# Performance work log

Measured on AMD Instinct MI355X. Metric: run time of the kernel, lower is better.

Reference implementation:

```python
import jax, jax.numpy as jnp
import numpy as np
import jax.scipy.linalg

BATCH = 1048576
M_NUM = 2
DT = 0.0166667
NN_RATIO = 0.5
SLOPE = 0.01  # torch LeakyReLU default negative_slope


def setup_inputs() -> dict:
    key = jax.random.key(0)
    ks = jax.random.split(key, 16)
    inp = {}
    inp["SS"] = jax.random.normal(ks[0], (BATCH, 2), dtype=jnp.float32)
    inp["Alphas"] = jax.random.uniform(ks[1], (BATCH, M_NUM), dtype=jnp.float32)
    # per-muscle scalar parameters (positive so sqrt(K*I) is valid)
    inp["K0s"] = jax.random.uniform(ks[2], (M_NUM,), minval=0.5, maxval=1.5)
    inp["K1s"] = jax.random.uniform(ks[3], (M_NUM,), minval=0.5, maxval=1.5)
    inp["L0s"] = jax.random.uniform(ks[4], (M_NUM,), minval=0.5, maxval=1.5)
    inp["L1s"] = jax.random.uniform(ks[5], (M_NUM,), minval=0.1, maxval=0.6)
    inp["Ms"] = jnp.array([1.0, -1.0], dtype=jnp.float32)  # moment arms
    inp["I_p"] = jnp.array([1.0], dtype=jnp.float32)
    inp["B_p"] = jnp.array([0.05], dtype=jnp.float32)
    inp["K_p"] = jnp.array([1.0], dtype=jnp.float32)
    # per-muscle compensational MLP weights: 3-32-32-32-1 (eval mode, dropout off)
    s = 0.1
    inp["W1"] = jax.random.normal(ks[6], (M_NUM, 3, 32)) * s
    inp["b1"] = jax.random.normal(ks[7], (M_NUM, 32)) * s
    inp["W2"] = jax.random.normal(ks[8], (M_NUM, 32, 32)) * s
    inp["b2"] = jax.random.normal(ks[9], (M_NUM, 32)) * s
    inp["W3"] = jax.random.normal(ks[10], (M_NUM, 32, 32)) * s
    inp["b3"] = jax.random.normal(ks[11], (M_NUM, 32)) * s
    inp["W4"] = jax.random.normal(ks[12], (M_NUM, 32, 1)) * s
    inp["b4"] = jax.random.normal(ks[13], (M_NUM, 1)) * s
    return inp


def _leaky(x):
    return jnp.where(x >= 0, x, SLOPE * x)


def reference(SS, Alphas, K0s, K1s, L0s, L1s, Ms, I_p, B_p, K_p,
              W1, b1, W2, b2, W3, b3, W4, b4):
    B = SS.shape[0]
    a = jnp.clip(Alphas, 0.0, 1.0)                      # (B, m)
    # muscle length / speed via scalar moment arms
    l = SS[:, 0:1] * Ms[None, :]                        # (B, m)
    dl = SS[:, 1:2] * Ms[None, :]                       # (B, m)
    # compensational MLPs, vectorized over muscles
    x = jnp.stack([l, dl, a], axis=-1)                  # (B, m, 3)
    h = _leaky(jnp.einsum('bmi,mio->bmo', x, W1) + b1[None])
    h = _leaky(jnp.einsum('bmi,mio->bmo', h, W2) + b2[None])
    h = _leaky(jnp.einsum('bmi,mio->bmo', h, W3) + b3[None])
    nn_out = jnp.tanh(jnp.einsum('bmi,mio->bmo', h, W4) + b4[None])[..., 0] * NN_RATIO  # (B, m)

    I0, B0p, K0p = I_p[0], B_p[0], K_p[0]
    K_m = K0s[None, :] + K1s[None, :] * a               # (B, m)
    K_tot = jnp.sum(K_m * Ms[None, :] ** 2, axis=1)     # (B,)
    A10 = -(K_tot + K0p) / I0
    D = 2.0 * jnp.sqrt(K_tot * I0)
    A11 = -(D + B0p) / I0
    B_F = K_m * (L0s[None, :] + L1s[None, :] * a - jnp.abs(l)) \
        + K1s[None, :] * L1s[None, :] * a * a * nn_out   # (B, m)
    B10 = jnp.sum(B_F * Ms[None, :], axis=1) / I0       # (B,)

    # Build block matrix M6 = [[A*dt, B*dt, 0], [0, 0, I2], [0, 0, 0]]
    M6 = jnp.zeros((B, 6, 6), dtype=SS.dtype)
    M6 = M6.at[:, 0, 1].set(DT)
    M6 = M6.at[:, 1, 0].set(A10 * DT)
    M6 = M6.at[:, 1, 1].set(A11 * DT)
    M6 = M6.at[:, 1, 2].set(B10 * DT)
    M6 = M6.at[:, 1, 3].set(DT / I0)
    M6 = M6.at[:, 2, 4].set(1.0)
    M6 = M6.at[:, 3, 5].set(1.0)

    expMT = jax.vmap(jax.scipy.linalg.expm)(M6)         # (B, 6, 6)
    Ad = expMT[:, :2, :2]
    Bd1 = expMT[:, :2, 4:6]
    Bd0 = expMT[:, :2, 2:4] - Bd1
    u = jnp.array([1.0, 0.0], dtype=SS.dtype)           # U0 = U1 = [1, 0]
    SSout = (jnp.einsum('bij,bj->bi', Ad, SS)
             + jnp.einsum('bij,j->bi', Bd0, u)
             + jnp.einsum('bij,j->bi', Bd1, u))          # (B, 2)
    return SSout[:, :1], SSout
```

## Files before the change

### kernel.cpp

```cpp
#include <hip/hip_runtime.h>
#include <hip/hip_bf16.h>

#define NTHREADS 256
#define WAVES    4
#define GPW      4
#define DT_F     0.0166667f

typedef _Float16 f16x8 __attribute__((ext_vector_type(8)));
typedef _Float16 f16x4 __attribute__((ext_vector_type(4)));
typedef _Float16 f16x2 __attribute__((ext_vector_type(2)));
typedef float    f32x4 __attribute__((ext_vector_type(4)));

#define BF16_PROBE 0xBF803F80u

#define A1T 0
#define A4T 1024
#define B2T 2048
#define B3T 3072
#define A2T 4096
#define A3T 6144
#define SMH_F16 8192

__device__ __forceinline__ float leaky(float x) { return fmaxf(x, 0.01f * x); }

__device__ __forceinline__ float tanh_fast(float x) {
    const float xc = fminf(fmaxf(x, -10.0f), 10.0f);
    const float t  = __expf(2.0f * xc);
    return (t - 1.0f) * __builtin_amdgcn_rcpf(t + 1.0f);
}

__device__ __forceinline__ f16x2 pkrtz(float a, float b) {
    return __builtin_bit_cast(f16x2, __builtin_amdgcn_cvt_pkrtz(a, b));
}

__device__ __forceinline__ f16x4 leaky_cvt(const f32x4 D) {
    f16x2 lo = pkrtz(D[0], D[1]);
    f16x2 hi = pkrtz(D[2], D[3]);
    const f16x2 sl = {(_Float16)0.01f, (_Float16)0.01f};
    lo = __builtin_elementwise_max(lo, lo * sl);
    hi = __builtin_elementwise_max(hi, hi * sl);
    return __builtin_shufflevector(lo, hi, 0, 1, 2, 3);
}

__device__ __forceinline__ f16x4 bias_leaky_cvt(const f32x4 D, const f16x4 b) {
    f16x2 lo = pkrtz(D[0], D[1]);
    f16x2 hi = pkrtz(D[2], D[3]);
    const f16x2 blo = {b[0], b[1]};
    const f16x2 bhi = {b[2], b[3]};
    lo = lo + blo;
    hi = hi + bhi;
    const f16x2 sl = {(_Float16)0.01f, (_Float16)0.01f};
    lo = __builtin_elementwise_max(lo, lo * sl);
    hi = __builtin_elementwise_max(hi, hi * sl);
    return __builtin_shufflevector(lo, hi, 0, 1, 2, 3);
}

__device__ __forceinline__ f16x8 concat8(const f16x4 a, const f16x4 b) {
    return __builtin_shufflevector(a, b, 0, 1, 2, 3, 4, 5, 6, 7);
}

__device__ __forceinline__ f32x4 mfma16(f16x4 a, f16x4 b, f32x4 c) {
    f32x4 d;
    asm("v_mfma_f32_16x16x16_f16 %0, %1, %2, %3"
        : "=&v"(d) : "v"(a), "v"(b), "v"(c));
    return d;
}
__device__ __forceinline__ f32x4 mfma32(f16x8 a, f16x8 b, f32x4 c) {
    f32x4 d;
    asm("v_mfma_f32_16x16x32_f16 %0, %1, %2, %3"
        : "=&v"(d) : "v"(a), "v"(b), "v"(c));
    return d;
}

__device__ __forceinline__ f16x4 ldsv4(const _Float16* p) {
    return *(const f16x4*)p;
}
__device__ __forceinline__ f16x8 ldsv8(const _Float16* p) {
    return *(const f16x8*)p;
}

__device__ __forceinline__ void epilogue_math(
    const float* P, float ss0, float ss1, float a0, float a1,
    float nn0, float nn1, float& o0f, float& o1f)
{
    const float K00 = P[0], K01 = P[1], K10 = P[2], K11 = P[3];
    const float L00 = P[4], L01 = P[5], L10 = P[6], L11 = P[7];
    const float Ms0 = P[8], Ms1 = P[9];
    const float I0  = P[10], B0p = P[11], K0p = P[12];

    const float Km0   = fmaf(K10, a0, K00);
    const float Km1   = fmaf(K11, a1, K01);
    const float K_tot = Km0*Ms0*Ms0 + Km1*Ms1*Ms1;
    const float invI  = 1.0f / I0;
    const float A10   = -(K_tot + K0p) * invI;
    const float Dd    = 2.0f * sqrtf(K_tot * I0);
    const float A11   = -(Dd + B0p) * invI;
    const float absl0 = fabsf(ss0 * Ms0);
    const float absl1 = fabsf(ss0 * Ms1);
    const float BF0   = Km0 * (L00 + L10*a0 - absl0) + K10*L10*a0*a0*nn0;
    const float BF1   = Km1 * (L01 + L11*a1 - absl1) + K11*L11*a1*a1*nn1;
    const float B10   = (BF0*Ms0 + BF1*Ms1) * invI;

    const float t01 = DT_F;
    const float t10 = A10 * DT_F;
    const float t11 = A11 * DT_F;

    float p00 = 1.0f/120.0f, p01 = 0.0f, p10 = 0.0f, p11 = 1.0f/120.0f;
    const float coef[4] = {1.0f/24.0f, 1.0f/6.0f, 0.5f, 1.0f};
    #pragma unroll
    for (int j = 0; j < 4; ++j) {
        const float cj  = coef[j];
        const float n00 = p01*t10 + cj;
        const float n01 = p00*t01 + p01*t11;
        const float n10 = p11*t10;
        const float n11 = p10*t01 + p11*t11 + cj;
        p00 = n00; p01 = n01; p10 = n10; p11 = n11;
    }
    const float e00 = 1.0f + t01*p10;
    const float e01 = t01*p11;
    const float e10 = t10*p00 + t11*p10;
    const float e11 = 1.0f + t10*p01 + t11*p11;

    const float cscale = DT_F * B10;
    o0f = fmaf(e00, ss0, fmaf(e01, ss1, p01 * cscale));
    o1f = fmaf(e10, ss0, fmaf(e11, ss1, p11 * cscale));
}

__device__ __forceinline__ float ldb(const __hip_bfloat16* p, int i) {
    return __bfloat162float(p[i]);
}

__device__ void run_bf16_fallback(
    const void* SSv, const void* ALv, const void* K0sv, const void* K1sv,
    const void* L0sv, const void* L1sv, const void* Msv, const void* I_pv,
    const void* B_pv, const void* K_pv, const void* W1v, const void* b1v,
    const void* W2v, const void* b2v, const void* W3v, const void* b3v,
    const void* W4v, const void* b4v, void* outv, int batch)
{
    const __hip_bfloat16* SS = (const __hip_bfloat16*)SSv;
    const __hip_bfloat16* AL = (const __hip_bfloat16*)ALv;
    const __hip_bfloat16* W1 = (const __hip_bfloat16*)W1v;
    const __hip_bfloat16* b1 = (const __hip_bfloat16*)b1v;
    const __hip_bfloat16* W2 = (const __hip_bfloat16*)W2v;
    const __hip_bfloat16* b2 = (const __hip_bfloat16*)b2v;
    const __hip_bfloat16* W3 = (const __hip_bfloat16*)W3v;
    const __hip_bfloat16* b3 = (const __hip_bfloat16*)b3v;
    const __hip_bfloat16* W4 = (const __hip_bfloat16*)W4v;
    const __hip_bfloat16* b4 = (const __hip_bfloat16*)b4v;

    float P[13];
    P[0] = ldb((const __hip_bfloat16*)K0sv, 0); P[1] = ldb((const __hip_bfloat16*)K0sv, 1);
    P[2] = ldb((const __hip_bfloat16*)K1sv, 0); P[3] = ldb((const __hip_bfloat16*)K1sv, 1);
    P[4] = ldb((const __hip_bfloat16*)L0sv, 0); P[5] = ldb((const __hip_bfloat16*)L0sv, 1);
    P[6] = ldb((const __hip_bfloat16*)L1sv, 0); P[7] = ldb((const __hip_bfloat16*)L1sv, 1);
    P[8] = ldb((const __hip_bfloat16*)Msv, 0);  P[9] = ldb((const __hip_bfloat16*)Msv, 1);
    P[10] = ldb((const __hip_bfloat16*)I_pv, 0);
    P[11] = ldb((const __hip_bfloat16*)B_pv, 0);
    P[12] = ldb((const __hip_bfloat16*)K_pv, 0);

    const int stride = gridDim.x * blockDim.x;
    for (int e = blockIdx.x * blockDim.x + threadIdx.x; e < batch; e += stride) {
        const float ss0 = ldb(SS, 2*e), ss1 = ldb(SS, 2*e+1);
        float a0 = fminf(fmaxf(ldb(AL, 2*e),   0.0f), 1.0f);
        float a1 = fminf(fmaxf(ldb(AL, 2*e+1), 0.0f), 1.0f);
        float nn[2];
        #pragma unroll 1
        for (int m = 0; m < 2; ++m) {
            const float am = m ? a1 : a0;
            const float l = ss0 * P[8+m], dl = ss1 * P[8+m];
            float h[32];
            #pragma unroll
            for (int o = 0; o < 32; ++o)
                h[o] = leaky(fmaf(l, ldb(W1, m*96+o),
                             fmaf(dl, ldb(W1, m*96+32+o),
                             fmaf(am, ldb(W1, m*96+64+o), ldb(b1, m*32+o)))));
            float g[32];
            #pragma unroll 1
            for (int oc = 0; oc < 4; ++oc) {
                float acc[8];
                #pragma unroll
                for (int j = 0; j < 8; ++j) acc[j] = ldb(b2, m*32+oc*8+j);
                #pragma unroll
                for (int k = 0; k < 32; ++k) {
                    #pragma unroll
                    for (int j = 0; j < 8; ++j)
                        acc[j] = fmaf(h[k], ldb(W2, m*1024+k*32+oc*8+j), acc[j]);
                }
                #pragma unroll
                for (int j = 0; j < 8; ++j) g[oc*8+j] = leaky(acc[j]);
            }
            float h3[32];
            #pragma unroll 1
            for (int oc = 0; oc < 4; ++oc) {
                float acc[8];
                #pragma unroll
                for (int j = 0; j < 8; ++j) acc[j] = ldb(b3, m*32+oc*8+j);
                #pragma unroll
                for (int k = 0; k < 32; ++k) {
                    #pragma unroll
                    for (int j = 0; j < 8; ++j)
                        acc[j] = fmaf(g[k], ldb(W3, m*1024+k*32+oc*8+j), acc[j]);
                }
                #pragma unroll
                for (int j = 0; j < 8; ++j) h3[oc*8+j] = leaky(acc[j]);
            }
            float acc = ldb(b4, m);
            #pragma unroll
            for (int k = 0; k < 32; ++k) acc = fmaf(h3[k], ldb(W4, m*32+k), acc);
            nn[m] = tanh_fast(acc) * 0.5f;
        }
        float o0f, o1f;
        epilogue_math(P, ss0, ss1, a0, a1, nn[0], nn[1], o0f, o1f);
        __hip_bfloat16* out0 = (__hip_bfloat16*)outv;
        __hip_bfloat162* out1 = (__hip_bfloat162*)(out0 + batch);
        out0[e] = __float2bfloat16(o0f);
        __hip_bfloat162 pr;
        pr.x = __float2bfloat16(o0f);
        pr.y = __float2bfloat16(o1f);
        out1[e] = pr;
    }
}

__global__ __launch_bounds__(NTHREADS, 4) void joint_kernel(
    const void* __restrict__ SSv, const void* __restrict__ ALv,
    const void* __restrict__ K0sv, const void* __restrict__ K1sv,
    const void* __restrict__ L0sv, const void* __restrict__ L1sv,
    const void* __restrict__ Msv,  const void* __restrict__ I_pv,
    const void* __restrict__ B_pv, const void* __restrict__ K_pv,
    const void* __restrict__ W1v,  const void* __restrict__ b1v,
    const void* __restrict__ W2v,  const void* __restrict__ b2v,
    const void* __restrict__ W3v,  const void* __restrict__ b3v,
    const void* __restrict__ W4v,  const void* __restrict__ b4v,
    void* __restrict__ outv, int batch)
{
    const unsigned probe = *(const unsigned*)Msv;
    if (probe == BF16_PROBE) {
        run_bf16_fallback(SSv, ALv, K0sv, K1sv, L0sv, L1sv, Msv, I_pv, B_pv,
                          K_pv, W1v, b1v, W2v, b2v, W3v, b3v, W4v, b4v,
                          outv, batch);
        return;
    }

    const float* SS = (const float*)SSv;
    const float* AL = (const float*)ALv;
    const float* W1 = (const float*)W1v;  const float* b1 = (const float*)b1v;
    const float* W2 = (const float*)W2v;  const float* b2 = (const float*)b2v;
    const float* W3 = (const float*)W3v;  const float* b3 = (const float*)b3v;
    const float* W4 = (const float*)W4v;  const float* b4 = (const float*)b4v;

    const int tid  = threadIdx.x;
    const int wave = tid >> 6;
    const int lane = tid & 63;
    const int n    = lane & 15;
    const int q    = lane >> 4;

    __shared__ __align__(16) _Float16 smh[SMH_F16];
    __shared__ float sb4[2];

    for (int i = tid; i < 2048; i += NTHREADS) {
        const int mi = i >> 10, rem = i & 1023, in = rem >> 5, out = rem & 31;
        const int qq = in >> 3, j = in & 7, h = (out >> 2) & 1;
        const int nn_ = ((out >> 3) << 2) | (out & 3);
        const int l  = (qq << 4) | nn_;
        smh[A2T + ((mi*2 + h)*64 + l)*8 + j] = (_Float16)W2[i];
        smh[A3T + ((mi*2 + h)*64 + l)*8 + j] = (_Float16)W3[i];
    }
    for (int i = tid; i < 1024; i += NTHREADS) {
        const int mi = i >> 9, h = (i >> 8) & 1, l = (i >> 2) & 63, j = i & 3;
        const int qq = l >> 4, nn_ = l & 15;
        const int gg = ((nn_ >> 2) << 3) + (nn_ & 3) + h*4;
        const int k  = qq*4 + j;
        float v = 0.0f;
        if (k < 3)       v = W1[mi*96 + k*32 + gg];
        else if (k == 3) v = b1[mi*32 + gg];
        smh[A1T + ((mi*2 + h)*64 + l)*4 + j] = (_Float16)v;
    }
    for (int i = tid; i < 1024; i += NTHREADS) {
        const int mi = i >> 9, l = (i >> 3) & 63, j = i & 7;
        smh[A4T + (mi*64 + l)*8 + j] = (_Float16)W4[mi*32 + (l >> 4)*8 + j];
    }
    for (int i = tid; i < 1024; i += NTHREADS) {
        const int mi = i >> 9, h = (i >> 8) & 1, l = (i >> 2) & 63, r = i & 3;
        smh[B2T + ((mi*2 + h)*64 + l)*4 + r] = (_Float16)b2[mi*32 + (l >> 4)*8 + h*4 + r];
        smh[B3T + ((mi*2 + h)*64 + l)*4 + r] = (_Float16)b3[mi*32 + (l >> 4)*8 + h*4 + r];
    }
    if (tid < 2) sb4[tid] = b4[tid];
    __syncthreads();

    f16x4 A1f[2][2], Bs2[2][2], Bs3[2][2];
    f16x8 A2f[2][2], A3f[2][2], A4f[2];
    #pragma unroll
    for (int mi = 0; mi < 2; ++mi) {
        #pragma unroll
        for (int h = 0; h < 2; ++h) {
            A1f[mi][h] = ldsv4(&smh[A1T + ((mi*2 + h)*64 + lane)*4]);
            A2f[mi][h] = ldsv8(&smh[A2T + ((mi*2 + h)*64 + lane)*8]);
            A3f[mi][h] = ldsv8(&smh[A3T + ((mi*2 + h)*64 + lane)*8]);
            Bs2[mi][h] = ldsv4(&smh[B2T + ((mi*2 + h)*64 + lane)*4]);
            Bs3[mi][h] = ldsv4(&smh[B3T + ((mi*2 + h)*64 + lane)*4]);
        }
        A4f[mi] = ldsv8(&smh[A4T + (mi*64 + lane)*8]);
    }
    const float b4s0 = sb4[0], b4s1 = sb4[1];

    float P[13];
    P[0]  = ((const float*)K0sv)[0]; P[1]  = ((const float*)K0sv)[1];
    P[2]  = ((const float*)K1sv)[0]; P[3]  = ((const float*)K1sv)[1];
    P[4]  = ((const float*)L0sv)[0]; P[5]  = ((const float*)L0sv)[1];
    P[6]  = ((const float*)L1sv)[0]; P[7]  = ((const float*)L1sv)[1];
    P[8]  = ((const float*)Msv)[0];  P[9]  = ((const float*)Msv)[1];
    P[10] = ((const float*)I_pv)[0];
    P[11] = ((const float*)B_pv)[0];
    P[12] = ((const float*)K_pv)[0];

    const f32x4 zero = {0.0f, 0.0f, 0.0f, 0.0f};
    const int groupBase = (blockIdx.x * WAVES + wave) * GPW;

    #pragma unroll 1
    for (int g = 0; g < GPW; ++g) {
        const int ebase = (groupBase + g) * 64;
        float my_r0 = 0.0f, my_r1 = 0.0f;

        float2 s0_, s1_, s2_, s3_, al0_, al1_, al2_, al3_;
        {
            const int e0 = min(ebase + 0*16 + n, batch - 1);
            const int e1 = min(ebase + 1*16 + n, batch - 1);
            const int e2 = min(ebase + 2*16 + n, batch - 1);
            const int e3 = min(ebase + 3*16 + n, batch - 1);
            s0_ = ((const float2*)SS)[e0]; al0_ = ((const float2*)AL)[e0];
            s1_ = ((const float2*)SS)[e1]; al1_ = ((const float2*)AL)[e1];
            s2_ = ((const float2*)SS)[e2]; al2_ = ((const float2*)AL)[e2];
            s3_ = ((const float2*)SS)[e3]; al3_ = ((const float2*)AL)[e3];
        }

        #pragma unroll 1
        for (int p = 0; p < 2; ++p) {
            float2 s[2], al[2];
            s[0]  = p ? s2_  : s0_;
            s[1]  = p ? s3_  : s1_;
            al[0] = p ? al2_ : al0_;
            al[1] = p ? al3_ : al1_;
            float a0c[2], a1c[2];
            #pragma unroll
            for (int ti = 0; ti < 2; ++ti) {
                a0c[ti] = fminf(fmaxf(al[ti].x, 0.0f), 1.0f);
                a1c[ti] = fminf(fmaxf(al[ti].y, 0.0f), 1.0f);
            }

            f16x4 B1[2][2];
            #pragma unroll
            for (int ti = 0; ti < 2; ++ti)
                #pragma unroll
                for (int mi = 0; mi < 2; ++mi) {
                    const float Msm = P[8 + mi];
                    const float am  = mi ? a1c[ti] : a0c[ti];
                    const f16x2 blo = pkrtz(s[ti].x * Msm, s[ti].y * Msm);
                    const f16x2 bhi = pkrtz(am, 1.0f);
                    B1[ti][mi] = __builtin_shufflevector(blo, bhi, 0, 1, 2, 3);
                }

            f16x8 Bx[2][2];
            #pragma unroll
            for (int ti = 0; ti < 2; ++ti)
                #pragma unroll
                for (int mi = 0; mi < 2; ++mi) {
                    const f32x4 d0 = mfma16(A1f[mi][0], B1[ti][mi], zero);
                    const f32x4 d1 = mfma16(A1f[mi][1], B1[ti][mi], zero);
                    Bx[ti][mi] = concat8(leaky_cvt(d0), leaky_cvt(d1));
                }
            #pragma unroll
            for (int ti = 0; ti < 2; ++ti)
                #pragma unroll
                for (int mi = 0; mi < 2; ++mi) {
                    const f32x4 d0 = mfma32(A2f[mi][0], Bx[ti][mi], zero);
                    const f32x4 d1 = mfma32(A2f[mi][1], Bx[ti][mi], zero);
                    Bx[ti][mi] = concat8(bias_leaky_cvt(d0, Bs2[mi][0]),
                                         bias_leaky_cvt(d1, Bs2[mi][1]));
                }
            #pragma unroll
            for (int ti = 0; ti < 2; ++ti)
                #pragma unroll
                for (int mi = 0; mi < 2; ++mi) {
                    const f32x4 d0 = mfma32(A3f[mi][0], Bx[ti][mi], zero);
                    const f32x4 d1 = mfma32(A3f[mi][1], Bx[ti][mi], zero);
                    Bx[ti][mi] = concat8(bias_leaky_cvt(d0, Bs3[mi][0]),
                                         bias_leaky_cvt(d1, Bs3[mi][1]));
                }
            #pragma unroll
            for (int ti = 0; ti < 2; ++ti) {
                const bool own = (q == (2*p + ti));
                #pragma unroll
                for (int mi = 0; mi < 2; ++mi) {
                    const f32x4 G = mfma32(A4f[mi], Bx[ti][mi], zero);
                    const float r = G[0] + (mi ? b4s1 : b4s0);
                    if (mi == 0) my_r0 = own ? r : my_r0;
                    else         my_r1 = own ? r : my_r1;
                }
            }
        }

        const int eo  = ebase + lane;
        const int eog = min(eo, batch - 1);
        const float2 se  = ((const float2*)SS)[eog];
        const float2 ale = ((const float2*)AL)[eog];
        const float a0 = fminf(fmaxf(ale.x, 0.0f), 1.0f);
        const float a1 = fminf(fmaxf(ale.y, 0.0f), 1.0f);
        const float nn0 = tanh_fast(my_r0) * 0.5f;
        const float nn1 = tanh_fast(my_r1) * 0.5f;
        float o0f, o1f;
        epilogue_math(P, se.x, se.y, a0, a1, nn0, nn1, o0f, o1f);
        if (eo < batch) {
            ((float*)outv)[eo] = o0f;
            ((float2*)((float*)outv + batch))[eo] = make_float2(o0f, o1f);
        }
    }
}

extern "C" void kernel_launch(void* const* d_in, const int* in_sizes, int n_in,
                              void* d_out, int out_size, void* d_ws, size_t ws_size,
                              hipStream_t stream) {
    const int batch = in_sizes[0] / 2;
    const int elemsPerBlock = 64 * GPW * WAVES;
    const int grid = (batch + elemsPerBlock - 1) / elemsPerBlock;
    joint_kernel<<<grid, NTHREADS, 0, stream>>>(
        d_in[0], d_in[1], d_in[2], d_in[3], d_in[4], d_in[5], d_in[6],
        d_in[7], d_in[8], d_in[9], d_in[10], d_in[11], d_in[12], d_in[13],
        d_in[14], d_in[15], d_in[16], d_in[17], d_out, batch);
}
```

Baseline: 121.9 us.

## Split per-muscle MLPs across wave pairs and exchange results via LDS

Each wave now evaluates the MLP for a single muscle instead of both, with pairs of waves sharing the same 64-element groups. The muscle-1 wave writes its result to a double-buffered LDS exchange, and after a block barrier the muscle-0 wave runs the epilogue and writes the output. This cuts per-wave register use (half the weight fragments), and launch bounds are raised to target higher occupancy. In exchange, the grid doubles, every block must redo the LDS weight staging, a block-wide sync is added per group, and half the waves sit idle during the epilogue.

```diff
diff --git a/kernel.cpp b/kernel.cpp
--- a/kernel.cpp
+++ b/kernel.cpp
@@ -221,7 +221,7 @@
     }
 }
 
-__global__ __launch_bounds__(NTHREADS, 4) void joint_kernel(
+__global__ __launch_bounds__(NTHREADS, 8) void joint_kernel(
     const void* __restrict__ SSv, const void* __restrict__ ALv,
     const void* __restrict__ K0sv, const void* __restrict__ K1sv,
     const void* __restrict__ L0sv, const void* __restrict__ L1sv,
@@ -253,55 +253,54 @@
     const int lane = tid & 63;
     const int n    = lane & 15;
     const int q    = lane >> 4;
+    const int mi   = wave & 1;
+    const int wp   = wave >> 1;
 
     __shared__ __align__(16) _Float16 smh[SMH_F16];
+    __shared__ float sxch[2][2][64];
     __shared__ float sb4[2];
 
     for (int i = tid; i < 2048; i += NTHREADS) {
-        const int mi = i >> 10, rem = i & 1023, in = rem >> 5, out = rem & 31;
+        const int mm = i >> 10, rem = i & 1023, in = rem >> 5, out = rem & 31;
         const int qq = in >> 3, j = in & 7, h = (out >> 2) & 1;
         const int nn_ = ((out >> 3) << 2) | (out & 3);
         const int l  = (qq << 4) | nn_;
-        smh[A2T + ((mi*2 + h)*64 + l)*8 + j] = (_Float16)W2[i];
-        smh[A3T + ((mi*2 + h)*64 + l)*8 + j] = (_Float16)W3[i];
+        smh[A2T + ((mm*2 + h)*64 + l)*8 + j] = (_Float16)W2[i];
+        smh[A3T + ((mm*2 + h)*64 + l)*8 + j] = (_Float16)W3[i];
     }
     for (int i = tid; i < 1024; i += NTHREADS) {
-        const int mi = i >> 9, h = (i >> 8) & 1, l = (i >> 2) & 63, j = i & 3;
+        const int mm = i >> 9, h = (i >> 8) & 1, l = (i >> 2) & 63, j = i & 3;
         const int qq = l >> 4, nn_ = l & 15;
         const int gg = ((nn_ >> 2) << 3) + (nn_ & 3) + h*4;
         const int k  = qq*4 + j;
         float v = 0.0f;
-        if (k < 3)       v = W1[mi*96 + k*32 + gg];
-        else if (k == 3) v = b1[mi*32 + gg];
-        smh[A1T + ((mi*2 + h)*64 + l)*4 + j] = (_Float16)v;
+        if (k < 3)       v = W1[mm*96 + k*32 + gg];
+        else if (k == 3) v = b1[mm*32 + gg];
+        smh[A1T + ((mm*2 + h)*64 + l)*4 + j] = (_Float16)v;
     }
     for (int i = tid; i < 1024; i += NTHREADS) {
-        const int mi = i >> 9, l = (i >> 3) & 63, j = i & 7;
-        smh[A4T + (mi*64 + l)*8 + j] = (_Float16)W4[mi*32 + (l >> 4)*8 + j];
+        const int mm = i >> 9, l = (i >> 3) & 63, j = i & 7;
+        smh[A4T + (mm*64 + l)*8 + j] = (_Float16)W4[mm*32 + (l >> 4)*8 + j];
     }
     for (int i = tid; i < 1024; i += NTHREADS) {
-        const int mi = i >> 9, h = (i >> 8) & 1, l = (i >> 2) & 63, r = i & 3;
-        smh[B2T + ((mi*2 + h)*64 + l)*4 + r] = (_Float16)b2[mi*32 + (l >> 4)*8 + h*4 + r];
-        smh[B3T + ((mi*2 + h)*64 + l)*4 + r] = (_Float16)b3[mi*32 + (l >> 4)*8 + h*4 + r];
+        const int mm = i >> 9, h = (i >> 8) & 1, l = (i >> 2) & 63, r = i & 3;
+        smh[B2T + ((mm*2 + h)*64 + l)*4 + r] = (_Float16)b2[mm*32 + (l >> 4)*8 + h*4 + r];
+        smh[B3T + ((mm*2 + h)*64 + l)*4 + r] = (_Float16)b3[mm*32 + (l >> 4)*8 + h*4 + r];
     }
     if (tid < 2) sb4[tid] = b4[tid];
     __syncthreads();
 
-    f16x4 A1f[2][2], Bs2[2][2], Bs3[2][2];
-    f16x8 A2f[2][2], A3f[2][2], A4f[2];
+    f16x4 A1f[2], Bs2[2], Bs3[2];
+    f16x8 A2f[2], A3f[2], A4f;
     #pragma unroll
-    for (int mi = 0; mi < 2; ++mi) {
-        #pragma unroll
-        for (int h = 0; h < 2; ++h) {
-            A1f[mi][h] = ldsv4(&smh[A1T + ((mi*2 + h)*64 + lane)*4]);
-            A2f[mi][h] = ldsv8(&smh[A2T + ((mi*2 + h)*64 + lane)*8]);
-            A3f[mi][h] = ldsv8(&smh[A3T + ((mi*2 + h)*64 + lane)*8]);
-            Bs2[mi][h] = ldsv4(&smh[B2T + ((mi*2 + h)*64 + lane)*4]);
-            Bs3[mi][h] = ldsv4(&smh[B3T + ((mi*2 + h)*64 + lane)*4]);
-        }
-        A4f[mi] = ldsv8(&smh[A4T + (mi*64 + lane)*8]);
-    }
-    const float b4s0 = sb4[0], b4s1 = sb4[1];
+    for (int h = 0; h < 2; ++h) {
+        A1f[h] = ldsv4(&smh[A1T + ((mi*2 + h)*64 + lane)*4]);
+        A2f[h] = ldsv8(&smh[A2T + ((mi*2 + h)*64 + lane)*8]);
+        A3f[h] = ldsv8(&smh[A3T + ((mi*2 + h)*64 + lane)*8]);
+        Bs2[h] = ldsv4(&smh[B2T + ((mi*2 + h)*64 + lane)*4]);
+        Bs3[h] = ldsv4(&smh[B3T + ((mi*2 + h)*64 + lane)*4]);
+    }
+    A4f = ldsv8(&smh[A4T + (mi*64 + lane)*8]);
 
     float P[13];
     P[0]  = ((const float*)K0sv)[0]; P[1]  = ((const float*)K0sv)[1];
@@ -313,105 +312,62 @@
     P[11] = ((const float*)B_pv)[0];
     P[12] = ((const float*)K_pv)[0];
 
+    const float Msm = mi ? P[9] : P[8];
+    const float b4s = mi ? sb4[1] : sb4[0];
+
     const f32x4 zero = {0.0f, 0.0f, 0.0f, 0.0f};
-    const int groupBase = (blockIdx.x * WAVES + wave) * GPW;
+    const int groupBase = (blockIdx.x * 2 + wp) * GPW;
 
     #pragma unroll 1
     for (int g = 0; g < GPW; ++g) {
         const int ebase = (groupBase + g) * 64;
-        float my_r0 = 0.0f, my_r1 = 0.0f;
-
-        float2 s0_, s1_, s2_, s3_, al0_, al1_, al2_, al3_;
-        {
-            const int e0 = min(ebase + 0*16 + n, batch - 1);
-            const int e1 = min(ebase + 1*16 + n, batch - 1);
-            const int e2 = min(ebase + 2*16 + n, batch - 1);
-            const int e3 = min(ebase + 3*16 + n, batch - 1);
-            s0_ = ((const float2*)SS)[e0]; al0_ = ((const float2*)AL)[e0];
-            s1_ = ((const float2*)SS)[e1]; al1_ = ((const float2*)AL)[e1];
-            s2_ = ((const float2*)SS)[e2]; al2_ = ((const float2*)AL)[e2];
-            s3_ = ((const float2*)SS)[e3]; al3_ = ((const float2*)AL)[e3];
+        float my_r = 0.0f;
+
+        #pragma unroll 1
+        for (int t = 0; t < 4; ++t) {
+            const int e  = min(ebase + t*16 + n, batch - 1);
+            const float2 s  = ((const float2*)SS)[e];
+            const float2 al = ((const float2*)AL)[e];
+            const float a   = fminf(fmaxf(mi ? al.y : al.x, 0.0f), 1.0f);
+
+            const f16x2 blo = pkrtz(s.x * Msm, s.y * Msm);
+            const f16x2 bhi = pkrtz(a, 1.0f);
+            const f16x4 B1 = __builtin_shufflevector(blo, bhi, 0, 1, 2, 3);
+
+            const f32x4 d0a = mfma16(A1f[0], B1, zero);
+            const f32x4 d1a = mfma16(A1f[1], B1, zero);
+            f16x8 Bx = concat8(leaky_cvt(d0a), leaky_cvt(d1a));
+            const f32x4 d0b = mfma32(A2f[0], Bx, zero);
+            const f32x4 d1b = mfma32(A2f[1], Bx, zero);
+            Bx = concat8(bias_leaky_cvt(d0b, Bs2[0]),
+                         bias_leaky_cvt(d1b, Bs2[1]));
+            const f32x4 d0c = mfma32(A3f[0], Bx, zero);
+            const f32x4 d1c = mfma32(A3f[1], Bx, zero);
+            Bx = concat8(bias_leaky_cvt(d0c, Bs3[0]),
+                         bias_leaky_cvt(d1c, Bs3[1]));
+            const f32x4 G = mfma32(A4f, Bx, zero);
+            const float r = G[0] + b4s;
+            my_r = (q == t) ? r : my_r;
         }
 
-        #pragma unroll 1
-        for (int p = 0; p < 2; ++p) {
-            float2 s[2], al[2];
-            s[0]  = p ? s2_  : s0_;
-            s[1]  = p ? s3_  : s1_;
-            al[0] = p ? al2_ : al0_;
-            al[1] = p ? al3_ : al1_;
-            float a0c[2], a1c[2];
-            #pragma unroll
-            for (int ti = 0; ti < 2; ++ti) {
-                a0c[ti] = fminf(fmaxf(al[ti].x, 0.0f), 1.0f);
-                a1c[ti] = fminf(fmaxf(al[ti].y, 0.0f), 1.0f);
+        if (mi == 1) sxch[g & 1][wp][lane] = my_r;
+        __syncthreads();
+        if (mi == 0) {
+            const float r1 = sxch[g & 1][wp][lane];
+            const int eo  = ebase + lane;
+            const int eog = min(eo, batch - 1);
+            const float2 se  = ((const float2*)SS)[eog];
+            const float2 ale = ((const float2*)AL)[eog];
+            const float a0 = fminf(fmaxf(ale.x, 0.0f), 1.0f);
+            const float a1 = fminf(fmaxf(ale.y, 0.0f), 1.0f);
+            const float nn0 = tanh_fast(my_r) * 0.5f;
+            const float nn1 = tanh_fast(r1)   * 0.5f;
+            float o0f, o1f;
+            epilogue_math(P, se.x, se.y, a0, a1, nn0, nn1, o0f, o1f);
+            if (eo < batch) {
+                ((float*)outv)[eo] = o0f;
+                ((float2*)((float*)outv + batch))[eo] = make_float2(o0f, o1f);
             }
-
-            f16x4 B1[2][2];
-            #pragma unroll
-            for (int ti = 0; ti < 2; ++ti)
-                #pragma unroll
-                for (int mi = 0; mi < 2; ++mi) {
-                    const float Msm = P[8 + mi];
-                    const float am  = mi ? a1c[ti] : a0c[ti];
-                    const f16x2 blo = pkrtz(s[ti].x * Msm, s[ti].y * Msm);
-                    const f16x2 bhi = pkrtz(am, 1.0f);
-                    B1[ti][mi] = __builtin_shufflevector(blo, bhi, 0, 1, 2, 3);
-                }
-
-            f16x8 Bx[2][2];
-            #pragma unroll
-            for (int ti = 0; ti < 2; ++ti)
-                #pragma unroll
-                for (int mi = 0; mi < 2; ++mi) {
-                    const f32x4 d0 = mfma16(A1f[mi][0], B1[ti][mi], zero);
-                    const f32x4 d1 = mfma16(A1f[mi][1], B1[ti][mi], zero);
-                    Bx[ti][mi] = concat8(leaky_cvt(d0), leaky_cvt(d1));
-                }
-            #pragma unroll
-            for (int ti = 0; ti < 2; ++ti)
-                #pragma unroll
-                for (int mi = 0; mi < 2; ++mi) {
-                    const f32x4 d0 = mfma32(A2f[mi][0], Bx[ti][mi], zero);
-                    const f32x4 d1 = mfma32(A2f[mi][1], Bx[ti][mi], zero);
-                    Bx[ti][mi] = concat8(bias_leaky_cvt(d0, Bs2[mi][0]),
-                                         bias_leaky_cvt(d1, Bs2[mi][1]));
-                }
-            #pragma unroll
-            for (int ti = 0; ti < 2; ++ti)
-                #pragma unroll
-                for (int mi = 0; mi < 2; ++mi) {
-                    const f32x4 d0 = mfma32(A3f[mi][0], Bx[ti][mi], zero);
-                    const f32x4 d1 = mfma32(A3f[mi][1], Bx[ti][mi], zero);
-                    Bx[ti][mi] = concat8(bias_leaky_cvt(d0, Bs3[mi][0]),
-                                         bias_leaky_cvt(d1, Bs3[mi][1]));
-                }
-            #pragma unroll
-            for (int ti = 0; ti < 2; ++ti) {
-                const bool own = (q == (2*p + ti));
-                #pragma unroll
-                for (int mi = 0; mi < 2; ++mi) {
-                    const f32x4 G = mfma32(A4f[mi], Bx[ti][mi], zero);
-                    const float r = G[0] + (mi ? b4s1 : b4s0);
-                    if (mi == 0) my_r0 = own ? r : my_r0;
-                    else         my_r1 = own ? r : my_r1;
-                }
-            }
-        }
-
-        const int eo  = ebase + lane;
-        const int eog = min(eo, batch - 1);
-        const float2 se  = ((const float2*)SS)[eog];
-        const float2 ale = ((const float2*)AL)[eog];
-        const float a0 = fminf(fmaxf(ale.x, 0.0f), 1.0f);
-        const float a1 = fminf(fmaxf(ale.y, 0.0f), 1.0f);
-        const float nn0 = tanh_fast(my_r0) * 0.5f;
-        const float nn1 = tanh_fast(my_r1) * 0.5f;
-        float o0f, o1f;
-        epilogue_math(P, se.x, se.y, a0, a1, nn0, nn1, o0f, o1f);
-        if (eo < batch) {
-            ((float*)outv)[eo] = o0f;
-            ((float2*)((float*)outv + batch))[eo] = make_float2(o0f, o1f);
         }
     }
 }
@@ -420,7 +376,7 @@
                               void* d_out, int out_size, void* d_ws, size_t ws_size,
                               hipStream_t stream) {
     const int batch = in_sizes[0] / 2;
-    const int elemsPerBlock = 64 * GPW * WAVES;
+    const int elemsPerBlock = 64 * GPW * 2;
     const int grid = (batch + elemsPerBlock - 1) / elemsPerBlock;
     joint_kernel<<<grid, NTHREADS, 0, stream>>>(
         d_in[0], d_in[1], d_in[2], d_in[3], d_in[4], d_in[5], d_in[6],
```

After: 138.1 us. 13.3% more time.
